# Kernel tuning notes

Measured on AMD Instinct MI355X. Metric: run time of the kernel, lower is better.

Reference implementation:

```python
import jax, jax.numpy as jnp
import numpy as np

B = 2097152
CXR, ECG, EHR = 15, 14, 13
TOTAL = CXR + ECG + EHR  # 42
LN_EPS = 1e-5


def setup_inputs() -> dict:
    key = jax.random.key(0)
    ks = jax.random.split(key, 40)
    f32 = jnp.float32
    inp = {
        "cxr_probs": jax.random.normal(ks[0], (B, CXR), dtype=f32),
        "ecg_probs": jax.random.normal(ks[1], (B, ECG), dtype=f32),
        "ehr_probs": jax.random.normal(ks[2], (B, EHR), dtype=f32),
    }
    for i, (name, E) in enumerate([("cxr", CXR), ("ecg", ECG), ("ehr", EHR)]):
        k0 = 3 + i * 8
        s_in = 1.0 / np.sqrt(E)
        s_kv = 1.0 / np.sqrt(TOTAL)
        inp[f"in_w_{name}"] = jax.random.normal(ks[k0], (3 * E, E), dtype=f32) * s_in
        inp[f"in_b_{name}"] = jnp.zeros((3 * E,), dtype=f32)
        inp[f"out_w_{name}"] = jax.random.normal(ks[k0 + 1], (E, E), dtype=f32) * s_in
        inp[f"out_b_{name}"] = jnp.zeros((E,), dtype=f32)
        inp[f"kv_w_{name}"] = jax.random.normal(ks[k0 + 2], (E, TOTAL), dtype=f32) * s_kv
        inp[f"kv_b_{name}"] = jax.random.normal(ks[k0 + 3], (E,), dtype=f32) * s_kv
        inp[f"ln_g_{name}"] = jnp.ones((E,), dtype=f32)
        inp[f"ln_b_{name}"] = jnp.zeros((E,), dtype=f32)
    return inp


def _branch(x, ctx, in_w, in_b, out_w, out_b, kv_w, kv_b, ln_g, ln_b):
    # x: [B, E], ctx: [B, 42]
    E = x.shape[-1]
    kv = ctx @ kv_w.T + kv_b                      # [B, E]
    # nn.MultiheadAttention with q_len = kv_len = 1: softmax over a single
    # key is identically 1, so attn_out == v_proj(kv) exactly.
    Wv, bv = in_w[2 * E:], in_b[2 * E:]
    v = kv @ Wv.T + bv                            # [B, E]
    attended = v @ out_w.T + out_b                # [B, E]
    y = x + attended
    mu = jnp.mean(y, axis=-1, keepdims=True)
    var = jnp.mean(jnp.square(y - mu), axis=-1, keepdims=True)
    return (y - mu) * jax.lax.rsqrt(var + LN_EPS) * ln_g + ln_b


def reference(cxr_probs, ecg_probs, ehr_probs,
              in_w_cxr, in_b_cxr, out_w_cxr, out_b_cxr, kv_w_cxr, kv_b_cxr, ln_g_cxr, ln_b_cxr,
              in_w_ecg, in_b_ecg, out_w_ecg, out_b_ecg, kv_w_ecg, kv_b_ecg, ln_g_ecg, ln_b_ecg,
              in_w_ehr, in_b_ehr, out_w_ehr, out_b_ehr, kv_w_ehr, kv_b_ehr, ln_g_ehr, ln_b_ehr):
    ctx = jnp.concatenate([cxr_probs, ecg_probs, ehr_probs], axis=1)  # [B, 42]
    cxr_out = _branch(cxr_probs, ctx, in_w_cxr, in_b_cxr, out_w_cxr, out_b_cxr,
                      kv_w_cxr, kv_b_cxr, ln_g_cxr, ln_b_cxr)
    ecg_out = _branch(ecg_probs, ctx, in_w_ecg, in_b_ecg, out_w_ecg, out_b_ecg,
                      kv_w_ecg, kv_b_ecg, ln_g_ecg, ln_b_ecg)
    ehr_out = _branch(ehr_probs, ctx, in_w_ehr, in_b_ehr, out_w_ehr, out_b_ehr,
                      kv_w_ehr, kv_b_ehr, ln_g_ehr, ln_b_ehr)
    return (cxr_out, ecg_out, ehr_out)
```

## Files before the change

kernel.cpp:

```cpp
#include <hip/hip_runtime.h>
#include <stdint.h>

constexpr int CXR = 15, ECG = 14, EHR = 13;
constexpr int TOTAL = 42;
constexpr int MPITCH = 44;
constexpr float LN_EPS = 1e-5f;

constexpr int WS_M    = 0;
constexpr int WS_B    = TOTAL * MPITCH;
constexpr int WS_G    = WS_B + TOTAL;
constexpr int WS_BETA = WS_G + TOTAL;
constexpr int WS_FLOATS = WS_BETA + TOTAL;

constexpr int ROWS = 256;
constexpr int S0 = 0;
constexpr int S1 = ROWS * CXR;
constexpr int S2 = S1 + ROWS * ECG;
constexpr int STAGE_FLOATS = S2 + ROWS * EHR;
constexpr int C0 = ROWS * CXR / 4;
constexpr int C1 = ROWS * ECG / 4;
constexpr int C2 = ROWS * EHR / 4;

typedef float f4v __attribute__((ext_vector_type(4)));
typedef __attribute__((address_space(4))) const f4v   CF4;
typedef __attribute__((address_space(4))) const float CFc;

__device__ __forceinline__ CF4* cast4(const float* p) {
    return (CF4*)(unsigned long long)p;
}
__device__ __forceinline__ CFc* cast1(const float* p) {
    return (CFc*)(unsigned long long)p;
}

struct FuseArgs {
    const float *in_w, *in_b, *out_w, *out_b, *kv_w, *kv_b, *ln_g, *ln_b;
    int E, R;
};

__global__ void fuse_weights_kernel(FuseArgs a0, FuseArgs a1, FuseArgs a2,
                                    float* __restrict__ ws) {
    FuseArgs a = (blockIdx.x == 0) ? a0 : (blockIdx.x == 1 ? a1 : a2);
    const int E = a.E, R = a.R;
    const int tid = threadIdx.x;

    __shared__ float T1[15 * 42];
    __shared__ float b1[15];

    for (int idx = tid; idx < E * TOTAL; idx += blockDim.x) {
        int i = idx / TOTAL, j = idx % TOTAL;
        float acc = 0.f;
        for (int k = 0; k < E; ++k)
            acc = fmaf(a.in_w[(2 * E + i) * E + k], a.kv_w[k * TOTAL + j], acc);
        T1[i * TOTAL + j] = acc;
    }
    if (tid < E) {
        float acc = a.in_b[2 * E + tid];
        for (int k = 0; k < E; ++k)
            acc = fmaf(a.in_w[(2 * E + tid) * E + k], a.kv_b[k], acc);
        b1[tid] = acc;
    }
    __syncthreads();

    for (int idx = tid; idx < E * MPITCH; idx += blockDim.x) {
        int i = idx / MPITCH, j = idx % MPITCH;
        float acc = 0.f;
        if (j < TOTAL)
            for (int k = 0; k < E; ++k)
                acc = fmaf(a.out_w[i * E + k], T1[k * TOTAL + j], acc);
        ws[WS_M + (R + i) * MPITCH + j] = acc;
    }
    if (tid < E) {
        float acc = a.out_b[tid];
        for (int k = 0; k < E; ++k)
            acc = fmaf(a.out_w[tid * E + k], b1[k], acc);
        ws[WS_B + R + tid]    = acc;
        ws[WS_G + R + tid]    = a.ln_g[tid];
        ws[WS_BETA + R + tid] = a.ln_b[tid];
    }
}

__device__ __forceinline__ void stage_seg(const float* __restrict__ g,
                                          float* sbase, int nchunks, int tid) {
    const int wbase = tid & ~63;
#pragma unroll
    for (int it = 0; it < 4; ++it) {
        int idx = tid + it * 256;
        if (idx < nchunks) {
            const __attribute__((address_space(1))) void* src =
                (const __attribute__((address_space(1))) void*)
                    ((const char*)g + (size_t)idx * 16);
            __attribute__((address_space(3))) void* dst =
                (__attribute__((address_space(3))) void*)
                    ((char*)sbase + (size_t)(wbase + it * 256) * 16);
            __builtin_amdgcn_global_load_lds(src, dst, 16, 0, 0);
        }
    }
}

template <int E, int R, int SBASE>
__device__ __forceinline__ void compute_seg(const float (&ctx)[MPITCH],
                                            const float* __restrict__ ws,
                                            float* __restrict__ sbuf, int tid) {
    float y[E];
#pragma unroll
    for (int i = 0; i < E; ++i) {
        CF4* wrow = cast4(ws + WS_M + (R + i) * MPITCH);
        float acc = *cast1(ws + WS_B + R + i);
#pragma unroll
        for (int q = 0; q < MPITCH / 4; ++q) {
            f4v w = wrow[q];
            acc = fmaf(w.x, ctx[4 * q + 0], acc);
            acc = fmaf(w.y, ctx[4 * q + 1], acc);
            acc = fmaf(w.z, ctx[4 * q + 2], acc);
            acc = fmaf(w.w, ctx[4 * q + 3], acc);
        }
        y[i] = ctx[R + i] + acc;
    }
    float mu = 0.f;
#pragma unroll
    for (int i = 0; i < E; ++i) mu += y[i];
    mu *= (1.0f / E);
    float var = 0.f;
#pragma unroll
    for (int i = 0; i < E; ++i) { float d = y[i] - mu; var = fmaf(d, d, var); }
    var *= (1.0f / E);
    float rs = rsqrtf(var + LN_EPS);
#pragma unroll
    for (int i = 0; i < E; ++i) {
        float n = (y[i] - mu) * rs;
        sbuf[SBASE + tid * E + i] = fmaf(n, *cast1(ws + WS_G + R + i),
                                         *cast1(ws + WS_BETA + R + i));
    }
}

__global__ __launch_bounds__(256) void cmca_main(
        const float* __restrict__ cxr, const float* __restrict__ ecg,
        const float* __restrict__ ehr, const float* __restrict__ ws,
        float* __restrict__ out_cxr, float* __restrict__ out_ecg,
        float* __restrict__ out_ehr) {
    __shared__ __align__(16) float sbuf[STAGE_FLOATS];
    float4* st4 = (float4*)sbuf;
    const int tid = threadIdx.x;
    const size_t tile = blockIdx.x;

    const float* g0 = cxr + tile * (size_t)(ROWS * CXR);
    const float* g1 = ecg + tile * (size_t)(ROWS * ECG);
    const float* g2 = ehr + tile * (size_t)(ROWS * EHR);

    stage_seg(g0, sbuf + S0, C0, tid);
    stage_seg(g1, sbuf + S1, C1, tid);
    stage_seg(g2, sbuf + S2, C2, tid);
    __syncthreads();

    float ctx[MPITCH];
#pragma unroll
    for (int j = 0; j < CXR; ++j) ctx[j] = sbuf[S0 + tid * CXR + j];
#pragma unroll
    for (int j = 0; j < ECG; ++j) ctx[CXR + j] = sbuf[S1 + tid * ECG + j];
#pragma unroll
    for (int j = 0; j < EHR; ++j) ctx[CXR + ECG + j] = sbuf[S2 + tid * EHR + j];
    __syncthreads();
    ctx[42] = 0.f;
    ctx[43] = 0.f;

    compute_seg<CXR, 0, S0>(ctx, ws, sbuf, tid);
    compute_seg<ECG, CXR, S1>(ctx, ws, sbuf, tid);
    compute_seg<EHR, CXR + ECG, S2>(ctx, ws, sbuf, tid);
    __syncthreads();

    float4* o0 = (float4*)(out_cxr + tile * (size_t)(ROWS * CXR));
    float4* o1 = (float4*)(out_ecg + tile * (size_t)(ROWS * ECG));
    float4* o2 = (float4*)(out_ehr + tile * (size_t)(ROWS * EHR));
#pragma unroll
    for (int it = 0; it < 4; ++it) {
        int idx = tid + it * 256;
        if (idx < C0) o0[idx] = st4[idx];
    }
#pragma unroll
    for (int it = 0; it < 4; ++it) {
        int idx = tid + it * 256;
        if (idx < C1) o1[idx] = st4[C0 + idx];
    }
#pragma unroll
    for (int it = 0; it < 4; ++it) {
        int idx = tid + it * 256;
        if (idx < C2) o2[idx] = st4[C0 + C1 + idx];
    }
}

extern "C" void kernel_launch(void* const* d_in, const int* in_sizes, int n_in,
                              void* d_out, int out_size, void* d_ws, size_t ws_size,
                              hipStream_t stream) {
    const float* cxr = (const float*)d_in[0];
    const float* ecg = (const float*)d_in[1];
    const float* ehr = (const float*)d_in[2];
    float* ws = (float*)d_ws;
    float* out = (float*)d_out;

    const size_t Bn = (size_t)in_sizes[0] / CXR;

    auto mk = [&](int base, int E, int R) {
        FuseArgs a;
        a.in_w  = (const float*)d_in[base + 0];
        a.in_b  = (const float*)d_in[base + 1];
        a.out_w = (const float*)d_in[base + 2];
        a.out_b = (const float*)d_in[base + 3];
        a.kv_w  = (const float*)d_in[base + 4];
        a.kv_b  = (const float*)d_in[base + 5];
        a.ln_g  = (const float*)d_in[base + 6];
        a.ln_b  = (const float*)d_in[base + 7];
        a.E = E; a.R = R;
        return a;
    };
    FuseArgs a0 = mk(3, CXR, 0);
    FuseArgs a1 = mk(11, ECG, CXR);
    FuseArgs a2 = mk(19, EHR, CXR + ECG);

    fuse_weights_kernel<<<3, 256, 0, stream>>>(a0, a1, a2, ws);

    const int tiles = (int)(Bn / ROWS);
    cmca_main<<<tiles, 256, 0, stream>>>(cxr, ecg, ehr, ws,
                                         out,
                                         out + Bn * CXR,
                                         out + Bn * (CXR + ECG));
}
```

Baseline: 176.7 us.

## Make each wavefront own a private LDS tile and drop block barriers

Reworks the main kernel so each 64-lane wavefront stages, computes and writes back its own 64-row tile in a private LDS region, using only a vmcnt wait instead of block-wide __syncthreads. Blocks shrink to 128 threads with smaller shared memory, and the 42-wide dot products switch to packed two-wide FMA (v_pk_fma) on float2 weight loads. The aim is to remove barrier stalls and to let more independent waves overlap memory and compute. The risks are a lost LDS write-to-read ordering guarantee, since no explicit barrier or lgkm wait follows the global_load_lds, more blocks to launch, and uncoalesced per-lane LDS reads.

Result: faster. 172.3 us (-2.5%).

```diff
diff --git a/kernel.cpp b/kernel.cpp
--- a/kernel.cpp
+++ b/kernel.cpp
@@ -12,21 +12,21 @@
 constexpr int WS_BETA = WS_G + TOTAL;
 constexpr int WS_FLOATS = WS_BETA + TOTAL;
 
-constexpr int ROWS = 256;
-constexpr int S0 = 0;
-constexpr int S1 = ROWS * CXR;
-constexpr int S2 = S1 + ROWS * ECG;
-constexpr int STAGE_FLOATS = S2 + ROWS * EHR;
-constexpr int C0 = ROWS * CXR / 4;
-constexpr int C1 = ROWS * ECG / 4;
-constexpr int C2 = ROWS * EHR / 4;
-
-typedef float f4v __attribute__((ext_vector_type(4)));
-typedef __attribute__((address_space(4))) const f4v   CF4;
+constexpr int WROWS = 64;
+constexpr int WFLOATS = WROWS * TOTAL;
+constexpr int WS0F = 0;
+constexpr int WS1F = WROWS * CXR;
+constexpr int WS2F = WS1F + WROWS * ECG;
+constexpr int WC0 = WROWS * CXR / 4;
+constexpr int WC1 = WROWS * ECG / 4;
+constexpr int WC2 = WROWS * EHR / 4;
+
+typedef float f2v __attribute__((ext_vector_type(2)));
+typedef __attribute__((address_space(4))) const f2v   CF2;
 typedef __attribute__((address_space(4))) const float CFc;
 
-__device__ __forceinline__ CF4* cast4(const float* p) {
-    return (CF4*)(unsigned long long)p;
+__device__ __forceinline__ CF2* cast2(const float* p) {
+    return (CF2*)(unsigned long long)p;
 }
 __device__ __forceinline__ CFc* cast1(const float* p) {
     return (CFc*)(unsigned long long)p;
@@ -79,42 +79,40 @@
     }
 }
 
-__device__ __forceinline__ void stage_seg(const float* __restrict__ g,
-                                          float* sbase, int nchunks, int tid) {
-    const int wbase = tid & ~63;
-#pragma unroll
-    for (int it = 0; it < 4; ++it) {
-        int idx = tid + it * 256;
-        if (idx < nchunks) {
+template <int CH>
+__device__ __forceinline__ void stage_wave(const float* __restrict__ g,
+                                           float* lds_seg_base, int lane) {
+#pragma unroll
+    for (int it = 0; it < (CH + 63) / 64; ++it) {
+        int idx = lane + it * 64;
+        if (idx < CH) {
             const __attribute__((address_space(1))) void* src =
                 (const __attribute__((address_space(1))) void*)
                     ((const char*)g + (size_t)idx * 16);
             __attribute__((address_space(3))) void* dst =
                 (__attribute__((address_space(3))) void*)
-                    ((char*)sbase + (size_t)(wbase + it * 256) * 16);
+                    ((char*)lds_seg_base + it * 1024);
             __builtin_amdgcn_global_load_lds(src, dst, 16, 0, 0);
         }
     }
 }
 
-template <int E, int R, int SBASE>
-__device__ __forceinline__ void compute_seg(const float (&ctx)[MPITCH],
+template <int E, int R, int SF>
+__device__ __forceinline__ void compute_seg(const f2v (&ctx2)[MPITCH / 2],
                                             const float* __restrict__ ws,
-                                            float* __restrict__ sbuf, int tid) {
+                                            float* __restrict__ wb, int lane) {
+    const float* ctxs = (const float*)ctx2;
     float y[E];
 #pragma unroll
     for (int i = 0; i < E; ++i) {
-        CF4* wrow = cast4(ws + WS_M + (R + i) * MPITCH);
-        float acc = *cast1(ws + WS_B + R + i);
-#pragma unroll
-        for (int q = 0; q < MPITCH / 4; ++q) {
-            f4v w = wrow[q];
-            acc = fmaf(w.x, ctx[4 * q + 0], acc);
-            acc = fmaf(w.y, ctx[4 * q + 1], acc);
-            acc = fmaf(w.z, ctx[4 * q + 2], acc);
-            acc = fmaf(w.w, ctx[4 * q + 3], acc);
+        CF2* wrow = cast2(ws + WS_M + (R + i) * MPITCH);
+        f2v acc = { *cast1(ws + WS_B + R + i), 0.f };
+#pragma unroll
+        for (int q = 0; q < MPITCH / 2; ++q) {
+            f2v w = wrow[q];
+            acc = __builtin_elementwise_fma(w, ctx2[q], acc);
         }
-        y[i] = ctx[R + i] + acc;
+        y[i] = ctxs[R + i] + acc.x + acc.y;
     }
     float mu = 0.f;
 #pragma unroll
@@ -128,63 +126,66 @@
 #pragma unroll
     for (int i = 0; i < E; ++i) {
         float n = (y[i] - mu) * rs;
-        sbuf[SBASE + tid * E + i] = fmaf(n, *cast1(ws + WS_G + R + i),
-                                         *cast1(ws + WS_BETA + R + i));
-    }
-}
-
-__global__ __launch_bounds__(256) void cmca_main(
+        wb[SF + lane * E + i] = fmaf(n, *cast1(ws + WS_G + R + i),
+                                     *cast1(ws + WS_BETA + R + i));
+    }
+}
+
+__global__ __launch_bounds__(128) void cmca_main(
         const float* __restrict__ cxr, const float* __restrict__ ecg,
         const float* __restrict__ ehr, const float* __restrict__ ws,
         float* __restrict__ out_cxr, float* __restrict__ out_ecg,
         float* __restrict__ out_ehr) {
-    __shared__ __align__(16) float sbuf[STAGE_FLOATS];
-    float4* st4 = (float4*)sbuf;
+    __shared__ __align__(16) float sbuf[2 * WFLOATS];
     const int tid = threadIdx.x;
-    const size_t tile = blockIdx.x;
-
-    const float* g0 = cxr + tile * (size_t)(ROWS * CXR);
-    const float* g1 = ecg + tile * (size_t)(ROWS * ECG);
-    const float* g2 = ehr + tile * (size_t)(ROWS * EHR);
-
-    stage_seg(g0, sbuf + S0, C0, tid);
-    stage_seg(g1, sbuf + S1, C1, tid);
-    stage_seg(g2, sbuf + S2, C2, tid);
-    __syncthreads();
-
-    float ctx[MPITCH];
-#pragma unroll
-    for (int j = 0; j < CXR; ++j) ctx[j] = sbuf[S0 + tid * CXR + j];
-#pragma unroll
-    for (int j = 0; j < ECG; ++j) ctx[CXR + j] = sbuf[S1 + tid * ECG + j];
-#pragma unroll
-    for (int j = 0; j < EHR; ++j) ctx[CXR + ECG + j] = sbuf[S2 + tid * EHR + j];
-    __syncthreads();
-    ctx[42] = 0.f;
-    ctx[43] = 0.f;
-
-    compute_seg<CXR, 0, S0>(ctx, ws, sbuf, tid);
-    compute_seg<ECG, CXR, S1>(ctx, ws, sbuf, tid);
-    compute_seg<EHR, CXR + ECG, S2>(ctx, ws, sbuf, tid);
-    __syncthreads();
-
-    float4* o0 = (float4*)(out_cxr + tile * (size_t)(ROWS * CXR));
-    float4* o1 = (float4*)(out_ecg + tile * (size_t)(ROWS * ECG));
-    float4* o2 = (float4*)(out_ehr + tile * (size_t)(ROWS * EHR));
+    const int w = tid >> 6;
+    const int lane = tid & 63;
+    const size_t gw = (size_t)blockIdx.x * 2 + w;
+
+    float* wb = sbuf + w * WFLOATS;
+
+    const float* g0 = cxr + gw * (size_t)(WROWS * CXR);
+    const float* g1 = ecg + gw * (size_t)(WROWS * ECG);
+    const float* g2 = ehr + gw * (size_t)(WROWS * EHR);
+
+    stage_wave<WC0>(g0, wb + WS0F, lane);
+    stage_wave<WC1>(g1, wb + WS1F, lane);
+    stage_wave<WC2>(g2, wb + WS2F, lane);
+    asm volatile("s_waitcnt vmcnt(0)" ::: "memory");
+
+    f2v ctx2[MPITCH / 2];
+    float* ctxs = (float*)ctx2;
+#pragma unroll
+    for (int j = 0; j < CXR; ++j) ctxs[j] = wb[WS0F + lane * CXR + j];
+#pragma unroll
+    for (int j = 0; j < ECG; ++j) ctxs[CXR + j] = wb[WS1F + lane * ECG + j];
+#pragma unroll
+    for (int j = 0; j < EHR; ++j) ctxs[CXR + ECG + j] = wb[WS2F + lane * EHR + j];
+    ctxs[42] = 0.f;
+    ctxs[43] = 0.f;
+
+    compute_seg<CXR, 0, WS0F>(ctx2, ws, wb, lane);
+    compute_seg<ECG, CXR, WS1F>(ctx2, ws, wb, lane);
+    compute_seg<EHR, CXR + ECG, WS2F>(ctx2, ws, wb, lane);
+
+    const float4* wb4 = (const float4*)wb;
+    float4* o0 = (float4*)(out_cxr + gw * (size_t)(WROWS * CXR));
+    float4* o1 = (float4*)(out_ecg + gw * (size_t)(WROWS * ECG));
+    float4* o2 = (float4*)(out_ehr + gw * (size_t)(WROWS * EHR));
 #pragma unroll
     for (int it = 0; it < 4; ++it) {
-        int idx = tid + it * 256;
-        if (idx < C0) o0[idx] = st4[idx];
+        int idx = lane + it * 64;
+        if (idx < WC0) o0[idx] = wb4[idx];
     }
 #pragma unroll
     for (int it = 0; it < 4; ++it) {
-        int idx = tid + it * 256;
-        if (idx < C1) o1[idx] = st4[C0 + idx];
+        int idx = lane + it * 64;
+        if (idx < WC1) o1[idx] = wb4[WC0 + idx];
     }
 #pragma unroll
     for (int it = 0; it < 4; ++it) {
-        int idx = tid + it * 256;
-        if (idx < C2) o2[idx] = st4[C0 + C1 + idx];
+        int idx = lane + it * 64;
+        if (idx < WC2) o2[idx] = wb4[WC0 + WC1 + idx];
     }
 }
 
@@ -218,9 +219,9 @@
 
     fuse_weights_kernel<<<3, 256, 0, stream>>>(a0, a1, a2, ws);
 
-    const int tiles = (int)(Bn / ROWS);
-    cmca_main<<<tiles, 256, 0, stream>>>(cxr, ecg, ehr, ws,
-                                         out,
-                                         out + Bn * CXR,
-                                         out + Bn * (CXR + ECG));
-}
+    const int nblocks = (int)(Bn / (WROWS * 2));
+    cmca_main<<<nblocks, 128, 0, stream>>>(cxr, ecg, ehr, ws,
+                                           out,
+                                           out + Bn * CXR,
+                                           out + Bn * (CXR + ECG));
+}
```
